# Kernel optimization log

Measured on AMD Instinct MI355X. Metric: run time of the kernel, lower is better.

## Reference

```python
import jax, jax.numpy as jnp
import numpy as np

N, F_IN, H, C, D, NH, L, FF = 4096, 256, 2, 64, 128, 4, 2, 2048
DEG = 32


def setup_inputs() -> dict:
    key = jax.random.key(0)
    ks = jax.random.split(key, 32)
    s = 0.05
    # graph: random edges + self loops (PyG GATConv adds self loops)
    src = jax.random.randint(ks[0], (N * DEG,), 0, N)
    dst = jax.random.randint(ks[1], (N * DEG,), 0, N)
    loop = jnp.arange(N)
    edge_index = jnp.stack([jnp.concatenate([src, loop]),
                            jnp.concatenate([dst, loop])]).astype(jnp.int64)
    inp = {
        'x': jax.random.normal(ks[2], (N, F_IN), jnp.float32),
        'edge_index': edge_index,
        'enc_w1': jax.random.normal(ks[3], (F_IN, 128), jnp.float32) * s,
        'enc_b1': jnp.zeros((128,), jnp.float32),
        'enc_w2': jax.random.normal(ks[4], (128, D), jnp.float32) * s,
        'enc_b2': jnp.zeros((D,), jnp.float32),
        'gat_w': jax.random.normal(ks[5], (D, H * C), jnp.float32) * s,
        'gat_asrc': jax.random.normal(ks[6], (H, C), jnp.float32) * s,
        'gat_adst': jax.random.normal(ks[7], (H, C), jnp.float32) * s,
        'gat_bias': jnp.zeros((H * C,), jnp.float32),
        't_wq': jax.random.normal(ks[8], (L, D, D), jnp.float32) * s,
        't_bq': jnp.zeros((L, D), jnp.float32),
        't_wk': jax.random.normal(ks[9], (L, D, D), jnp.float32) * s,
        't_bk': jnp.zeros((L, D), jnp.float32),
        't_wv': jax.random.normal(ks[10], (L, D, D), jnp.float32) * s,
        't_bv': jnp.zeros((L, D), jnp.float32),
        't_wo': jax.random.normal(ks[11], (L, D, D), jnp.float32) * s,
        't_bo': jnp.zeros((L, D), jnp.float32),
        't_ln1_g': jnp.ones((L, D), jnp.float32),
        't_ln1_b': jnp.zeros((L, D), jnp.float32),
        't_ln2_g': jnp.ones((L, D), jnp.float32),
        't_ln2_b': jnp.zeros((L, D), jnp.float32),
        't_w1': jax.random.normal(ks[12], (L, D, FF), jnp.float32) * s,
        't_b1': jnp.zeros((L, FF), jnp.float32),
        't_w2': jax.random.normal(ks[13], (L, FF, D), jnp.float32) * s,
        't_b2': jnp.zeros((L, D), jnp.float32),
    }
    return inp


def _layer_norm(v, g, b):
    m = v.mean(-1, keepdims=True)
    var = v.var(-1, keepdims=True)
    return (v - m) / jnp.sqrt(var + 1e-5) * g + b


def _forward(x, edge_index, enc_w1, enc_b1, enc_w2, enc_b2,
             gat_w, gat_asrc, gat_adst, gat_bias,
             t_wq, t_bq, t_wk, t_bk, t_wv, t_bv, t_wo, t_bo,
             t_ln1_g, t_ln1_b, t_ln2_g, t_ln2_b, t_w1, t_b1, t_w2, t_b2):
    n = x.shape[0]
    # encoder MLP: Linear -> ReLU -> Linear
    h = jnp.maximum(x @ enc_w1 + enc_b1, 0.0) @ enc_w2 + enc_b2  # [N, D]
    # GATConv (concat heads), dropout inactive (eval)
    heads, ch = gat_asrc.shape
    hh = (h @ gat_w).reshape(n, heads, ch)                       # [N, H, C]
    src, dst = edge_index[0], edge_index[1]
    a_src = (hh * gat_asrc).sum(-1)                              # [N, H]
    a_dst = (hh * gat_adst).sum(-1)
    e = jax.nn.leaky_relu(a_src[src] + a_dst[dst], 0.2)          # [E, H]
    # segment softmax over destination nodes
    e_max = jax.ops.segment_max(e, dst, num_segments=n)
    e_exp = jnp.exp(e - e_max[dst])
    denom = jax.ops.segment_sum(e_exp, dst, num_segments=n)
    alpha = e_exp / denom[dst]                                   # [E, H]
    agg = jax.ops.segment_sum(alpha[:, :, None] * hh[src], dst, num_segments=n)
    y = agg.reshape(n, heads * ch) + gat_bias                    # [N, D]
    # TransformerEncoder (post-LN, relu FFN), unbatched sequence of N nodes
    d = y.shape[-1]
    dh = d // NH
    for l in range(t_wq.shape[0]):
        q = (y @ t_wq[l] + t_bq[l]).reshape(n, NH, dh)
        k = (y @ t_wk[l] + t_bk[l]).reshape(n, NH, dh)
        v = (y @ t_wv[l] + t_bv[l]).reshape(n, NH, dh)
        scores = jnp.einsum('nhd,mhd->hnm', q, k) / jnp.sqrt(jnp.float32(dh))
        p = jax.nn.softmax(scores, axis=-1)
        a = jnp.einsum('hnm,mhd->nhd', p, v).reshape(n, d)
        a = a @ t_wo[l] + t_bo[l]
        y = _layer_norm(y + a, t_ln1_g[l], t_ln1_b[l])
        f = jnp.maximum(y @ t_w1[l] + t_b1[l], 0.0) @ t_w2[l] + t_b2[l]
        y = _layer_norm(y + f, t_ln2_g[l], t_ln2_b[l])
    return y


def reference(x, edge_index, enc_w1, enc_b1, enc_w2, enc_b2,
              gat_w, gat_asrc, gat_adst, gat_bias,
              t_wq, t_bq, t_wk, t_bk, t_wv, t_bv, t_wo, t_bo,
              t_ln1_g, t_ln1_b, t_ln2_g, t_ln2_b, t_w1, t_b1, t_w2, t_b2):
    return _forward(x, edge_index, enc_w1, enc_b1, enc_w2, enc_b2,
                    gat_w, gat_asrc, gat_adst, gat_bias,
                    t_wq, t_bq, t_wk, t_bk, t_wv, t_bv, t_wo, t_bo,
                    t_ln1_g, t_ln1_b, t_ln2_g, t_ln2_b, t_w1, t_b1, t_w2, t_b2)
```

## Files before the change

kernel.cpp:

```cpp
#include <hip/hip_runtime.h>

typedef unsigned short u16;
typedef unsigned int u32;
typedef __attribute__((ext_vector_type(8))) short bh8;
typedef __attribute__((ext_vector_type(4))) float fx4;
typedef __attribute__((ext_vector_type(4))) short s4;
typedef __attribute__((ext_vector_type(2))) unsigned int u32x2;

#define QS 0.2550437194342803f

__device__ __forceinline__ u16 f2bf(float f) {
    unsigned u = __float_as_uint(f);
    u += 0x7fffu + ((u >> 16) & 1u);
    return (u16)(u >> 16);
}

__device__ __forceinline__ u32 cvtpk(float lo, float hi) {
    u32 r;
    asm("v_cvt_pk_bf16_f32 %0, %1, %2" : "=v"(r) : "v"(lo), "v"(hi));
    return r;
}

__global__ __launch_bounds__(256) void prep_kernel(
    const float* x, const float* ew1, const float* ew2, const float* gw,
    const float* wq, const float* wk, const float* wv, const float* wo,
    const float* w1, const float* w2,
    const float* bq, const float* bk, const float* bv,
    u16* xb, u16* ew1t, u16* ew2t, u16* gwt,
    u16* wqkvt, float* bqkv, u16* wot, u16* w1t, u16* w2t)
{
    __shared__ u16 tile[64 * 65];
    int bid = blockIdx.x;
    const int t = threadIdx.x;

    if (bid < 128) {
        const float4* x4 = (const float4*)x;
        s4* o4 = (s4*)xb;
        #pragma unroll
        for (int i = 0; i < 8; i++) {
            int fi = bid * 2048 + i * 256 + t;
            float4 v = x4[fi];
            s4 o = { (short)f2bf(v.x), (short)f2bf(v.y), (short)f2bf(v.z), (short)f2bf(v.w) };
            o4[fi] = o;
        }
        return;
    }
    bid -= 128;
    if (bid < 1) {
        for (int idx = t; idx < 768; idx += 256) {
            int l = idx / 384, n = idx % 384;
            float v;
            if (n < 128)      v = bq[l * 128 + n] * QS;
            else if (n < 256) v = bk[l * 128 + n - 128];
            else              v = bv[l * 128 + n - 256];
            bqkv[idx] = v;
        }
        return;
    }
    bid -= 1;

    const float* src; u16* dst; int R, C, tr, tc; float sc = 1.f;
    if (bid < 8)            { src = ew1; dst = ew1t; R = 256; C = 128; tr = bid >> 1; tc = bid & 1; }
    else if ((bid -= 8) < 4)  { src = ew2; dst = ew2t; R = 128; C = 128; tr = bid >> 1; tc = bid & 1; }
    else if ((bid -= 4) < 4)  { src = gw;  dst = gwt;  R = 128; C = 128; tr = bid >> 1; tc = bid & 1; }
    else if ((bid -= 4) < 24) {
        int l = bid / 12, r2 = bid % 12, which = r2 >> 2, i = r2 & 3;
        R = 128; C = 128; tr = i >> 1; tc = i & 1;
        if (which == 0)      { src = wq + l * 16384; dst = wqkvt + l * 49152;         sc = QS; }
        else if (which == 1) { src = wk + l * 16384; dst = wqkvt + l * 49152 + 16384; }
        else                 { src = wv + l * 16384; dst = wqkvt + l * 49152 + 32768; }
    }
    else if ((bid -= 24) < 8)   { int l = bid >> 2, i = bid & 3;  src = wo + l * 16384; dst = wot + l * 16384; R = 128; C = 128; tr = i >> 1; tc = i & 1; }
    else if ((bid -= 8) < 128)  { int l = bid >> 6, i = bid & 63; src = w1 + (size_t)l * 262144; dst = w1t + (size_t)l * 262144; R = 128;  C = 2048; tr = i & 1;  tc = i >> 1; }
    else { bid -= 128;            int l = bid >> 6, i = bid & 63; src = w2 + (size_t)l * 262144; dst = w2t + (size_t)l * 262144; R = 2048; C = 128;  tr = i >> 1; tc = i & 1; }

    const int r = t >> 2, cs = (t & 3) * 16;
    const float* sp = src + (size_t)(tr * 64 + r) * C + tc * 64 + cs;
    #pragma unroll
    for (int j = 0; j < 16; j++) tile[r * 65 + cs + j] = f2bf(sp[j] * sc);
    __syncthreads();
    u16* dp = dst + (size_t)(tc * 64 + r) * R + tr * 64 + cs;
    #pragma unroll
    for (int j = 0; j < 16; j++) dp[j] = tile[(cs + j) * 65 + r];
}

__global__ __launch_bounds__(256) void gemm_bf16(
    const u16* __restrict__ A, const u16* __restrict__ Bt,
    const float* __restrict__ bias,
    float* __restrict__ Cf, u16* __restrict__ Cb, float* __restrict__ Cpart,
    u16* __restrict__ Cvt,
    int M, int N, int K, int relu, int kchunk, int ldc)
{
    __shared__ __align__(16) u16 As[2][64][40];
    __shared__ __align__(16) u16 Bs[2][64][40];
    const int m0 = blockIdx.x * 64, n0 = blockIdx.y * 64, z = blockIdx.z;
    const int tid = threadIdx.x;
    const int lane = tid & 63, w = tid >> 6;
    const int wm = (w >> 1) * 32, wn = (w & 1) * 32;
    const int l15 = lane & 15, l4 = lane >> 4;
    const int srow = tid >> 2, skq = (tid & 3) * 8;
    const int k0 = z * kchunk;

    const u16* Ap = A + (size_t)(m0 + srow) * K + k0 + skq;
    const u16* Bp = Bt + (size_t)(n0 + srow) * K + k0 + skq;

    fx4 acc00 = {0,0,0,0}, acc01 = {0,0,0,0}, acc10 = {0,0,0,0}, acc11 = {0,0,0,0};

    *(int4*)&As[0][srow][skq] = *(const int4*)Ap;
    *(int4*)&Bs[0][srow][skq] = *(const int4*)Bp;

    const int niter = kchunk >> 5;
    for (int it = 0; it < niter; it++) {
        const int cur = it & 1;
        int4 ar, br;
        __syncthreads();
        if (it + 1 < niter) {
            ar = *(const int4*)(Ap + (it + 1) * 32);
            br = *(const int4*)(Bp + (it + 1) * 32);
        }
        bh8 a0 = *(const bh8*)&As[cur][wm + l15][l4 * 8];
        bh8 a1 = *(const bh8*)&As[cur][wm + 16 + l15][l4 * 8];
        bh8 b0 = *(const bh8*)&Bs[cur][wn + l15][l4 * 8];
        bh8 b1 = *(const bh8*)&Bs[cur][wn + 16 + l15][l4 * 8];
        acc00 = __builtin_amdgcn_mfma_f32_16x16x32_bf16(a0, b0, acc00, 0, 0, 0);
        acc01 = __builtin_amdgcn_mfma_f32_16x16x32_bf16(a0, b1, acc01, 0, 0, 0);
        acc10 = __builtin_amdgcn_mfma_f32_16x16x32_bf16(a1, b0, acc10, 0, 0, 0);
        acc11 = __builtin_amdgcn_mfma_f32_16x16x32_bf16(a1, b1, acc11, 0, 0, 0);
        if (it + 1 < niter) {
            *(int4*)&As[cur ^ 1][srow][skq] = ar;
            *(int4*)&Bs[cur ^ 1][srow][skq] = br;
        }
    }

    fx4* accs[2][2] = {{&acc00, &acc01}, {&acc10, &acc11}};
    #pragma unroll
    for (int i = 0; i < 2; i++)
        #pragma unroll
        for (int j = 0; j < 2; j++) {
            int colg = n0 + wn + j * 16 + l15;
            int rowb = m0 + wm + i * 16 + l4 * 4;
            if (Cpart) {
                float* cp = Cpart + (size_t)z * M * N;
                #pragma unroll
                for (int r = 0; r < 4; r++)
                    cp[(size_t)(rowb + r) * N + colg] = (*accs[i][j])[r];
                continue;
            }
            float bvv = bias ? bias[colg] : 0.f;
            float vals[4];
            #pragma unroll
            for (int r = 0; r < 4; r++) {
                float v = (*accs[i][j])[r] + bvv;
                vals[r] = relu ? fmaxf(v, 0.f) : v;
            }
            if (Cvt && colg >= 256) {
                s4 pk = { (short)f2bf(vals[0]), (short)f2bf(vals[1]),
                          (short)f2bf(vals[2]), (short)f2bf(vals[3]) };
                *(s4*)&Cvt[(size_t)(colg - 256) * 4096 + rowb] = pk;
            } else {
                #pragma unroll
                for (int r = 0; r < 4; r++) {
                    if (Cf) Cf[(size_t)(rowb + r) * ldc + colg] = vals[r];
                    if (Cb) Cb[(size_t)(rowb + r) * ldc + colg] = f2bf(vals[r]);
                }
            }
        }
}

__global__ __launch_bounds__(128) void gat_prep(
    const float* __restrict__ hh, const float* __restrict__ asrc,
    const float* __restrict__ adst, float* __restrict__ an_src,
    float* __restrict__ an_dst)
{
    int n = blockIdx.x, tid = threadIdx.x;
    int head = tid >> 6, c = tid & 63;
    float v = hh[n * 128 + tid];
    float ps = v * asrc[head * 64 + c];
    float pd = v * adst[head * 64 + c];
    for (int off = 32; off; off >>= 1) { ps += __shfl_down(ps, off); pd += __shfl_down(pd, off); }
    if (c == 0) { an_src[n * 2 + head] = ps; an_dst[n * 2 + head] = pd; }
}

__global__ void count_edges(const int* __restrict__ dst, int* counts, int E) {
    int i = blockIdx.x * 256 + threadIdx.x;
    if (i < E) atomicAdd(&counts[dst[i]], 1);
}

__global__ __launch_bounds__(1024) void scan_kernel(const int* __restrict__ counts,
                                                    int* row_start, int* cursor) {
    __shared__ int s[1024];
    int tid = threadIdx.x, b = tid * 4;
    int c0 = counts[b], c1 = counts[b+1], c2 = counts[b+2], c3 = counts[b+3];
    int sum = c0 + c1 + c2 + c3;
    s[tid] = sum;
    __syncthreads();
    for (int off = 1; off < 1024; off <<= 1) {
        int v = (tid >= off) ? s[tid - off] : 0;
        __syncthreads();
        s[tid] += v;
        __syncthreads();
    }
    int excl = s[tid] - sum;
    int r0 = excl, r1 = excl + c0, r2 = r1 + c1, r3 = r2 + c2;
    row_start[b] = r0; row_start[b+1] = r1; row_start[b+2] = r2; row_start[b+3] = r3;
    cursor[b] = r0; cursor[b+1] = r1; cursor[b+2] = r2; cursor[b+3] = r3;
    if (tid == 1023) row_start[4096] = s[1023];
}

__global__ void scatter_edges(const int* __restrict__ src, const int* __restrict__ dst,
                              int* cursor, int* csr_src, int E) {
    int i = blockIdx.x * 256 + threadIdx.x;
    if (i < E) { int pos = atomicAdd(&cursor[dst[i]], 1); csr_src[pos] = src[i]; }
}

__global__ __launch_bounds__(256) void gat_aggregate(
    const int* __restrict__ row_start, const int* __restrict__ csr_src,
    const float* __restrict__ an_src, const float* __restrict__ an_dst,
    const float* __restrict__ hh, const float* __restrict__ gbias,
    float* __restrict__ y32, u16* __restrict__ yb)
{
    int n = blockIdx.x, tid = threadIdx.x;
    const int lane = tid & 63, wv = tid >> 6;
    int start = row_start[n], end = row_start[n + 1];
    float ad0 = an_dst[n * 2 + 0], ad1 = an_dst[n * 2 + 1];
    __shared__ float rmx[4][2], rsm[4][2];
    __shared__ float sal0[128], sal1[128], sagg[256];
    __shared__ int sidx[128];

    float mx0 = -1e30f, mx1 = -1e30f;
    for (int i = start + tid; i < end; i += 256) {
        int s = csr_src[i];
        float e0 = an_src[s * 2 + 0] + ad0; e0 = e0 > 0.f ? e0 : 0.2f * e0;
        float e1 = an_src[s * 2 + 1] + ad1; e1 = e1 > 0.f ? e1 : 0.2f * e1;
        mx0 = fmaxf(mx0, e0); mx1 = fmaxf(mx1, e1);
    }
    for (int off = 32; off; off >>= 1) { mx0 = fmaxf(mx0, __shfl_down(mx0, off)); mx1 = fmaxf(mx1, __shfl_down(mx1, off)); }
    if (lane == 0) { rmx[wv][0] = mx0; rmx[wv][1] = mx1; }
    __syncthreads();
    mx0 = fmaxf(fmaxf(rmx[0][0], rmx[1][0]), fmaxf(rmx[2][0], rmx[3][0]));
    mx1 = fmaxf(fmaxf(rmx[0][1], rmx[1][1]), fmaxf(rmx[2][1], rmx[3][1]));

    float den0 = 0.f, den1 = 0.f;
    for (int i = start + tid; i < end; i += 256) {
        int s = csr_src[i];
        float e0 = an_src[s * 2 + 0] + ad0; e0 = e0 > 0.f ? e0 : 0.2f * e0;
        float e1 = an_src[s * 2 + 1] + ad1; e1 = e1 > 0.f ? e1 : 0.2f * e1;
        den0 += __expf(e0 - mx0); den1 += __expf(e1 - mx1);
    }
    for (int off = 32; off; off >>= 1) { den0 += __shfl_down(den0, off); den1 += __shfl_down(den1, off); }
    if (lane == 0) { rsm[wv][0] = den0; rsm[wv][1] = den1; }
    __syncthreads();
    den0 = rsm[0][0] + rsm[1][0] + rsm[2][0] + rsm[3][0];
    den1 = rsm[0][1] + rsm[1][1] + rsm[2][1] + rsm[3][1];
    float rd0 = 1.f / den0, rd1 = 1.f / den1;

    const int grp = tid >> 7, ch = tid & 127, head = ch >> 6;
    float agg = 0.f;
    for (int c0 = start; c0 < end; c0 += 128) {
        int cnt = min(128, end - c0);
        __syncthreads();
        if (tid < cnt) {
            int s = csr_src[c0 + tid];
            float e0 = an_src[s * 2 + 0] + ad0; e0 = e0 > 0.f ? e0 : 0.2f * e0;
            float e1 = an_src[s * 2 + 1] + ad1; e1 = e1 > 0.f ? e1 : 0.2f * e1;
            sal0[tid] = __expf(e0 - mx0) * rd0;
            sal1[tid] = __expf(e1 - mx1) * rd1;
            sidx[tid] = s;
        }
        __syncthreads();
        const float* sal = head ? sal1 : sal0;
        for (int j = grp; j < cnt; j += 2)
            agg += sal[j] * hh[(size_t)sidx[j] * 128 + ch];
    }
    sagg[tid] = agg;
    __syncthreads();
    if (tid < 128) {
        float v = sagg[tid] + sagg[tid + 128] + gbias[tid];
        y32[(size_t)n * 128 + tid] = v;
        yb[(size_t)n * 128 + tid] = f2bf(v);
    }
}

__global__ __launch_bounds__(256) void flash_attn_part(
    const u16* __restrict__ q, const u16* __restrict__ k,
    const u16* __restrict__ vt, float* __restrict__ po,
    float* __restrict__ pm, float* __restrict__ pl)
{
    __shared__ __align__(16) u16 Kb[2][64][40];
    __shared__ __align__(16) u16 Vb[2][32][72];
    __shared__ __align__(16) u16 Ps[4][16][72];
    const int q0 = blockIdx.x * 64, h = blockIdx.y, ch = blockIdx.z;
    const int tid = threadIdx.x;
    const int w = tid >> 6, lane = tid & 63, l15 = lane & 15, l4 = lane >> 4;

    bh8 qf = *(const bh8*)&q[(size_t)(q0 + w * 16 + l15) * 256 + h * 32 + l4 * 8];

    const int skey = tid >> 2, sds = (tid & 3) * 8;
    const int svd = tid >> 3, svk = (tid & 7) * 8;
    const u16* kgp = &k[(size_t)(ch * 512 + skey) * 256 + h * 32 + sds];
    const u16* vgp = &vt[(size_t)(h * 32 + svd) * 4096 + ch * 512 + svk];

    fx4 o0 = {0,0,0,0}, o1 = {0,0,0,0};
    float M = -1e30f, L = 0.f;

    *(int4*)&Kb[0][skey][sds] = *(const int4*)kgp;
    *(int4*)&Vb[0][svd][svk] = *(const int4*)vgp;

    for (int ti = 0; ti < 8; ti++) {
        const int cur = ti & 1;
        int4 kr, vr;
        __syncthreads();
        if (ti < 7) {
            kr = *(const int4*)(kgp + (size_t)(ti + 1) * 64 * 256);
            vr = *(const int4*)(vgp + (ti + 1) * 64);
        }

        fx4 s[4];
        #pragma unroll
        for (int sub = 0; sub < 4; sub++) {
            bh8 kf = *(const bh8*)&Kb[cur][sub * 16 + l15][l4 * 8];
            fx4 z = {0,0,0,0};
            s[sub] = __builtin_amdgcn_mfma_f32_16x16x32_bf16(kf, qf, z, 0, 0, 0);
        }
        float t0 = fmaxf(fmaxf(s[0][0], s[0][1]), s[0][2]);
        float t1 = fmaxf(fmaxf(s[0][3], s[1][0]), s[1][1]);
        float t2 = fmaxf(fmaxf(s[1][2], s[1][3]), s[2][0]);
        float t3 = fmaxf(fmaxf(s[2][1], s[2][2]), s[2][3]);
        float t4 = fmaxf(fmaxf(s[3][0], s[3][1]), s[3][2]);
        float pmax = fmaxf(fmaxf(fmaxf(t0, t1), t2), fmaxf(fmaxf(t3, t4), s[3][3]));
        pmax = fmaxf(pmax, __shfl_xor(pmax, 16));
        pmax = fmaxf(pmax, __shfl_xor(pmax, 32));
        if (!__all(pmax - M <= 8.0f)) {
            float f = __builtin_amdgcn_exp2f(M - pmax);
            M = pmax;
            o0 *= f; o1 *= f; L *= f;
        }

        #pragma unroll
        for (int sub = 0; sub < 4; sub++)
            #pragma unroll
            for (int r = 0; r < 4; r++)
                s[sub][r] = __builtin_amdgcn_exp2f(s[sub][r] - M);
        float ss0 = (s[0][0] + s[0][1]) + (s[0][2] + s[0][3]);
        float ss1 = (s[1][0] + s[1][1]) + (s[1][2] + s[1][3]);
        float ss2 = (s[2][0] + s[2][1]) + (s[2][2] + s[2][3]);
        float ss3 = (s[3][0] + s[3][1]) + (s[3][2] + s[3][3]);
        float lsum = (ss0 + ss1) + (ss2 + ss3);
        lsum += __shfl_xor(lsum, 16);
        lsum += __shfl_xor(lsum, 32);
        L += lsum;

        #pragma unroll
        for (int sub = 0; sub < 4; sub++) {
            u32x2 pk = { cvtpk(s[sub][0], s[sub][1]), cvtpk(s[sub][2], s[sub][3]) };
            *(u32x2*)&Ps[w][l15][sub * 16 + l4 * 4] = pk;
        }

        #pragma unroll
        for (int kc = 0; kc < 2; kc++) {
            bh8 bf  = *(const bh8*)&Ps[w][l15][kc * 32 + l4 * 8];
            bh8 af0 = *(const bh8*)&Vb[cur][l15][kc * 32 + l4 * 8];
            bh8 af1 = *(const bh8*)&Vb[cur][16 + l15][kc * 32 + l4 * 8];
            o0 = __builtin_amdgcn_mfma_f32_16x16x32_bf16(af0, bf, o0, 0, 0, 0);
            o1 = __builtin_amdgcn_mfma_f32_16x16x32_bf16(af1, bf, o1, 0, 0, 0);
        }

        if (ti < 7) {
            *(int4*)&Kb[cur ^ 1][skey][sds] = kr;
            *(int4*)&Vb[cur ^ 1][svd][svk] = vr;
        }
    }
    const int base = (blockIdx.x * 4 + h) * 8 + ch;
    const int qrow = w * 16 + l15;
    *(fx4*)&po[(size_t)(base * 64 + qrow) * 32 + l4 * 4]      = o0;
    *(fx4*)&po[(size_t)(base * 64 + qrow) * 32 + 16 + l4 * 4] = o1;
    if (l4 == 0) { pm[base * 64 + qrow] = M; pl[base * 64 + qrow] = L; }
}

__global__ __launch_bounds__(256) void attn_combine(
    const float* __restrict__ po, const float* __restrict__ pm,
    const float* __restrict__ pl, u16* __restrict__ out)
{
    int qb = blockIdx.x, h = blockIdx.y;
    int col = threadIdx.x & 31, r0 = threadIdx.x >> 5;
    int rb = (qb * 4 + h) * 8;
    for (int j = 0; j < 8; j++) {
        int row = r0 * 8 + j;
        float m = -1e30f;
        for (int c = 0; c < 8; c++) m = fmaxf(m, pm[(rb + c) * 64 + row]);
        float l = 0.f, o = 0.f;
        for (int c = 0; c < 8; c++) {
            float wgt = __builtin_amdgcn_exp2f(pm[(rb + c) * 64 + row] - m);
            l += wgt * pl[(rb + c) * 64 + row];
            o += wgt * po[(size_t)((rb + c) * 64 + row) * 32 + col];
        }
        out[(size_t)(qb * 64 + row) * 128 + h * 32 + col] = f2bf(o / l);
    }
}

__global__ __launch_bounds__(128) void add_ln(
    const float* __restrict__ y, const float* __restrict__ delta,
    const float* __restrict__ g, const float* __restrict__ b,
    float* __restrict__ out32, u16* __restrict__ outb)
{
    int n = blockIdx.x, tid = threadIdx.x;
    float v = y[(size_t)n * 128 + tid] + delta[(size_t)n * 128 + tid];
    float sacc = v;
    for (int off = 32; off; off >>= 1) sacc += __shfl_down(sacc, off);
    __shared__ float sm[2], sv[2];
    if ((tid & 63) == 0) sm[tid >> 6] = sacc;
    __syncthreads();
    float mean = (sm[0] + sm[1]) * (1.f / 128.f);
    float d = v - mean;
    float qacc = d * d;
    for (int off = 32; off; off >>= 1) qacc += __shfl_down(qacc, off);
    if ((tid & 63) == 0) sv[tid >> 6] = qacc;
    __syncthreads();
    float var = (sv[0] + sv[1]) * (1.f / 128.f);
    float o = d * rsqrtf(var + 1e-5f) * g[tid] + b[tid];
    out32[(size_t)n * 128 + tid] = o;
    outb[(size_t)n * 128 + tid] = f2bf(o);
}

__global__ __launch_bounds__(128) void add_ln8(
    const float* __restrict__ y, const float* __restrict__ part,
    const float* __restrict__ bias,
    const float* __restrict__ g, const float* __restrict__ b,
    float* __restrict__ out32, u16* __restrict__ outb)
{
    int n = blockIdx.x, tid = threadIdx.x;
    float v = y[(size_t)n * 128 + tid] + bias[tid];
    for (int z = 0; z < 8; z++) v += part[(size_t)z * 524288 + n * 128 + tid];
    float sacc = v;
    for (int off = 32; off; off >>= 1) sacc += __shfl_down(sacc, off);
    __shared__ float sm[2], sv[2];
    if ((tid & 63) == 0) sm[tid >> 6] = sacc;
    __syncthreads();
    float mean = (sm[0] + sm[1]) * (1.f / 128.f);
    float d = v - mean;
    float qacc = d * d;
    for (int off = 32; off; off >>= 1) qacc += __shfl_down(qacc, off);
    if ((tid & 63) == 0) sv[tid >> 6] = qacc;
    __syncthreads();
    float var = (sv[0] + sv[1]) * (1.f / 128.f);
    float o = d * rsqrtf(var + 1e-5f) * g[tid] + b[tid];
    out32[(size_t)n * 128 + tid] = o;
    outb[(size_t)n * 128 + tid] = f2bf(o);
}

extern "C" void kernel_launch(void* const* d_in, const int* in_sizes, int n_in,
                              void* d_out, int out_size, void* d_ws, size_t ws_size,
                              hipStream_t stream)
{
    const float* x     = (const float*)d_in[0];
    const int*   ei    = (const int*)  d_in[1];
    const float* ew1   = (const float*)d_in[2];
    const float* eb1   = (const float*)d_in[3];
    const float* ew2   = (const float*)d_in[4];
    const float* eb2   = (const float*)d_in[5];
    const float* gw    = (const float*)d_in[6];
    const float* gasrc = (const float*)d_in[7];
    const float* gadst = (const float*)d_in[8];
    const float* gbias = (const float*)d_in[9];
    const float* wq    = (const float*)d_in[10];
    const float* bq    = (const float*)d_in[11];
    const float* wk    = (const float*)d_in[12];
    const float* bk    = (const float*)d_in[13];
    const float* wv    = (const float*)d_in[14];
    const float* bv    = (const float*)d_in[15];
    const float* wo    = (const float*)d_in[16];
    const float* bo    = (const float*)d_in[17];
    const float* ln1g  = (const float*)d_in[18];
    const float* ln1b  = (const float*)d_in[19];
    const float* ln2g  = (const float*)d_in[20];
    const float* ln2b  = (const float*)d_in[21];
    const float* w1    = (const float*)d_in[22];
    const float* b1    = (const float*)d_in[23];
    const float* w2    = (const float*)d_in[24];
    const float* b2    = (const float*)d_in[25];

    const int E = in_sizes[1] / 2;
    const int* esrc = ei;
    const int* edst = ei + E;

    char* p = (char*)d_ws;
    auto alloc = [&](size_t bytes) -> void* {
        void* r = (void*)p;
        p += (bytes + 255) & ~(size_t)255;
        return r;
    };
    u16* xb    = (u16*)alloc(4096 * 256 * 2);
    u16* ew1t  = (u16*)alloc(128 * 256 * 2);
    u16* ew2t  = (u16*)alloc(128 * 128 * 2);
    u16* gwt   = (u16*)alloc(128 * 128 * 2);
    u16* wqkvt = (u16*)alloc(2 * 384 * 128 * 2);
    float* bqkv = (float*)alloc(2 * 384 * 4);
    u16* wot   = (u16*)alloc(2 * 128 * 128 * 2);
    u16* w1t   = (u16*)alloc(2 * 2048 * 128 * 2);
    u16* w2t   = (u16*)alloc(2 * 128 * 2048 * 2);
    u16* h1b   = (u16*)alloc(4096 * 128 * 2);
    u16* hb    = (u16*)alloc(4096 * 128 * 2);
    float* hh  = (float*)alloc(4096 * 128 * 4);
    float* ansrc = (float*)alloc(4096 * 2 * 4);
    float* andst = (float*)alloc(4096 * 2 * 4);
    int* counts    = (int*)alloc(4096 * 4);
    int* row_start = (int*)alloc(4097 * 4);
    int* cursor    = (int*)alloc(4096 * 4);
    int* csr_src   = (int*)alloc((size_t)E * 4);
    float* y32 = (float*)alloc(4096 * 128 * 4);
    u16* yb    = (u16*)alloc(4096 * 128 * 2);
    u16* qkvb  = (u16*)alloc((size_t)4096 * 256 * 2);
    u16* vtb   = (u16*)alloc(4096 * 128 * 2);
    u16* attnb = (u16*)alloc(4096 * 128 * 2);
    float* po  = (float*)alloc((size_t)64 * 4 * 8 * 64 * 32 * 4);
    float* pm  = (float*)alloc(64 * 4 * 8 * 64 * 4);
    float* pl  = (float*)alloc(64 * 4 * 8 * 64 * 4);
    float* proj32 = (float*)alloc(4096 * 128 * 4);
    u16* ff1b  = (u16*)alloc((size_t)4096 * 2048 * 2);
    float* ff2part = (float*)alloc((size_t)8 * 4096 * 128 * 4);

    prep_kernel<<<433, 256, 0, stream>>>(x, ew1, ew2, gw, wq, wk, wv, wo, w1, w2,
                                         bq, bk, bv,
                                         xb, ew1t, ew2t, gwt, wqkvt, bqkv, wot, w1t, w2t);

    gemm_bf16<<<dim3(64, 2), 256, 0, stream>>>(xb, ew1t, eb1, nullptr, h1b, nullptr, nullptr, 4096, 128, 256, 1, 256, 128);
    gemm_bf16<<<dim3(64, 2), 256, 0, stream>>>(h1b, ew2t, eb2, nullptr, hb, nullptr, nullptr, 4096, 128, 128, 0, 128, 128);

    gemm_bf16<<<dim3(64, 2), 256, 0, stream>>>(hb, gwt, nullptr, hh, nullptr, nullptr, nullptr, 4096, 128, 128, 0, 128, 128);
    gat_prep<<<4096, 128, 0, stream>>>(hh, gasrc, gadst, ansrc, andst);
    hipMemsetAsync(counts, 0, 4096 * sizeof(int), stream);
    count_edges<<<(E + 255) / 256, 256, 0, stream>>>(edst, counts, E);
    scan_kernel<<<1, 1024, 0, stream>>>(counts, row_start, cursor);
    scatter_edges<<<(E + 255) / 256, 256, 0, stream>>>(esrc, edst, cursor, csr_src, E);
    gat_aggregate<<<4096, 256, 0, stream>>>(row_start, csr_src, ansrc, andst, hh, gbias, y32, yb);

    for (int l = 0; l < 2; l++) {
        gemm_bf16<<<dim3(64, 6), 256, 0, stream>>>(yb, wqkvt + l * 49152, bqkv + l * 384, nullptr, qkvb, nullptr, vtb, 4096, 384, 128, 0, 128, 256);
        flash_attn_part<<<dim3(64, 4, 8), 256, 0, stream>>>(qkvb, qkvb + 128, vtb, po, pm, pl);
        attn_combine<<<dim3(64, 4), 256, 0, stream>>>(po, pm, pl, attnb);
        gemm_bf16<<<dim3(64, 2), 256, 0, stream>>>(attnb, wot + l * 16384, bo + l * 128, proj32, nullptr, nullptr, nullptr, 4096, 128, 128, 0, 128, 128);
        add_ln<<<4096, 128, 0, stream>>>(y32, proj32, ln1g + l * 128, ln1b + l * 128, y32, yb);
        gemm_bf16<<<dim3(64, 32), 256, 0, stream>>>(yb, w1t + (size_t)l * 262144, b1 + l * 2048, nullptr, ff1b, nullptr, nullptr, 4096, 2048, 128, 1, 128, 2048);
        gemm_bf16<<<dim3(64, 2, 8), 256, 0, stream>>>(ff1b, w2t + (size_t)l * 262144, nullptr, nullptr, nullptr, ff2part, nullptr, 4096, 128, 2048, 0, 256, 128);
        float* outp = (l == 1) ? (float*)d_out : y32;
        add_ln8<<<4096, 128, 0, stream>>>(y32, ff2part, b2 + l * 128, ln2g + l * 128, ln2b + l * 128, outp, yb);
    }
}
```

Before: 209.8 us.

## Use wave-shuffle scan and halve flash attention key tile to 32

The scan kernel replaces its shared-memory Hillis-Steele loop, which needed many block barriers, with an intra-wave shuffle scan plus a small per-wave sum table and a single barrier. The flash attention partial kernel now processes 32 keys per iteration instead of 64 and runs twice as many iterations, using 8-byte global loads and smaller LDS buffers. This shrinks LDS footprint and register pressure, which may allow more resident blocks. In exchange it doubles the per-tile overhead: barriers, softmax max/sum shuffles and rescale checks.

```diff
diff --git a/kernel.cpp b/kernel.cpp
--- a/kernel.cpp
+++ b/kernel.cpp
@@ -188,23 +188,30 @@
 
 __global__ __launch_bounds__(1024) void scan_kernel(const int* __restrict__ counts,
                                                     int* row_start, int* cursor) {
-    __shared__ int s[1024];
-    int tid = threadIdx.x, b = tid * 4;
+    __shared__ int wsum[16];
+    int tid = threadIdx.x, lane = tid & 63, wv = tid >> 6;
+    int b = tid * 4;
     int c0 = counts[b], c1 = counts[b+1], c2 = counts[b+2], c3 = counts[b+3];
     int sum = c0 + c1 + c2 + c3;
-    s[tid] = sum;
-    __syncthreads();
-    for (int off = 1; off < 1024; off <<= 1) {
-        int v = (tid >= off) ? s[tid - off] : 0;
-        __syncthreads();
-        s[tid] += v;
-        __syncthreads();
-    }
-    int excl = s[tid] - sum;
+    int inc = sum;
+    #pragma unroll
+    for (int off = 1; off < 64; off <<= 1) {
+        int v = __shfl_up(inc, off);
+        if (lane >= off) inc += v;
+    }
+    if (lane == 63) wsum[wv] = inc;
+    __syncthreads();
+    int base = 0;
+    #pragma unroll
+    for (int i = 0; i < 16; i++) {
+        int v = wsum[i];
+        base += (i < wv) ? v : 0;
+    }
+    int excl = base + inc - sum;
     int r0 = excl, r1 = excl + c0, r2 = r1 + c1, r3 = r2 + c2;
     row_start[b] = r0; row_start[b+1] = r1; row_start[b+2] = r2; row_start[b+3] = r3;
     cursor[b] = r0; cursor[b+1] = r1; cursor[b+2] = r2; cursor[b+3] = r3;
-    if (tid == 1023) row_start[4096] = s[1023];
+    if (tid == 1023) row_start[4096] = base + inc;
 }
 
 __global__ void scatter_edges(const int* __restrict__ src, const int* __restrict__ dst,
@@ -286,48 +293,45 @@
     const u16* __restrict__ vt, float* __restrict__ po,
     float* __restrict__ pm, float* __restrict__ pl)
 {
-    __shared__ __align__(16) u16 Kb[2][64][40];
-    __shared__ __align__(16) u16 Vb[2][32][72];
-    __shared__ __align__(16) u16 Ps[4][16][72];
+    __shared__ __align__(16) u16 Kb[2][32][40];
+    __shared__ __align__(16) u16 Vb[2][32][40];
+    __shared__ __align__(16) u16 Ps[4][16][40];
     const int q0 = blockIdx.x * 64, h = blockIdx.y, ch = blockIdx.z;
     const int tid = threadIdx.x;
     const int w = tid >> 6, lane = tid & 63, l15 = lane & 15, l4 = lane >> 4;
 
     bh8 qf = *(const bh8*)&q[(size_t)(q0 + w * 16 + l15) * 256 + h * 32 + l4 * 8];
 
-    const int skey = tid >> 2, sds = (tid & 3) * 8;
-    const int svd = tid >> 3, svk = (tid & 7) * 8;
+    const int skey = tid >> 3, sds = (tid & 7) * 4;
+    const int svd = tid >> 3, svk = (tid & 7) * 4;
     const u16* kgp = &k[(size_t)(ch * 512 + skey) * 256 + h * 32 + sds];
     const u16* vgp = &vt[(size_t)(h * 32 + svd) * 4096 + ch * 512 + svk];
 
     fx4 o0 = {0,0,0,0}, o1 = {0,0,0,0};
     float M = -1e30f, L = 0.f;
 
-    *(int4*)&Kb[0][skey][sds] = *(const int4*)kgp;
-    *(int4*)&Vb[0][svd][svk] = *(const int4*)vgp;
-
-    for (int ti = 0; ti < 8; ti++) {
+    *(int2*)&Kb[0][skey][sds] = *(const int2*)kgp;
+    *(int2*)&Vb[0][svd][svk] = *(const int2*)vgp;
+
+    for (int ti = 0; ti < 16; ti++) {
         const int cur = ti & 1;
-        int4 kr, vr;
+        int2 kr, vr;
         __syncthreads();
-        if (ti < 7) {
-            kr = *(const int4*)(kgp + (size_t)(ti + 1) * 64 * 256);
-            vr = *(const int4*)(vgp + (ti + 1) * 64);
-        }
-
-        fx4 s[4];
+        if (ti < 15) {
+            kr = *(const int2*)(kgp + (size_t)(ti + 1) * 32 * 256);
+            vr = *(const int2*)(vgp + (ti + 1) * 32);
+        }
+
+        fx4 s[2];
         #pragma unroll
-        for (int sub = 0; sub < 4; sub++) {
+        for (int sub = 0; sub < 2; sub++) {
             bh8 kf = *(const bh8*)&Kb[cur][sub * 16 + l15][l4 * 8];
             fx4 z = {0,0,0,0};
             s[sub] = __builtin_amdgcn_mfma_f32_16x16x32_bf16(kf, qf, z, 0, 0, 0);
         }
-        float t0 = fmaxf(fmaxf(s[0][0], s[0][1]), s[0][2]);
-        float t1 = fmaxf(fmaxf(s[0][3], s[1][0]), s[1][1]);
-        float t2 = fmaxf(fmaxf(s[1][2], s[1][3]), s[2][0]);
-        float t3 = fmaxf(fmaxf(s[2][1], s[2][2]), s[2][3]);
-        float t4 = fmaxf(fmaxf(s[3][0], s[3][1]), s[3][2]);
-        float pmax = fmaxf(fmaxf(fmaxf(t0, t1), t2), fmaxf(fmaxf(t3, t4), s[3][3]));
+        float m0 = fmaxf(fmaxf(s[0][0], s[0][1]), fmaxf(s[0][2], s[0][3]));
+        float m1 = fmaxf(fmaxf(s[1][0], s[1][1]), fmaxf(s[1][2], s[1][3]));
+        float pmax = fmaxf(m0, m1);
         pmax = fmaxf(pmax, __shfl_xor(pmax, 16));
         pmax = fmaxf(pmax, __shfl_xor(pmax, 32));
         if (!__all(pmax - M <= 8.0f)) {
@@ -337,37 +341,34 @@
         }
 
         #pragma unroll
-        for (int sub = 0; sub < 4; sub++)
+        for (int sub = 0; sub < 2; sub++)
             #pragma unroll
             for (int r = 0; r < 4; r++)
                 s[sub][r] = __builtin_amdgcn_exp2f(s[sub][r] - M);
         float ss0 = (s[0][0] + s[0][1]) + (s[0][2] + s[0][3]);
         float ss1 = (s[1][0] + s[1][1]) + (s[1][2] + s[1][3]);
-        float ss2 = (s[2][0] + s[2][1]) + (s[2][2] + s[2][3]);
-        float ss3 = (s[3][0] + s[3][1]) + (s[3][2] + s[3][3]);
-        float lsum = (ss0 + ss1) + (ss2 + ss3);
+        float lsum = ss0 + ss1;
         lsum += __shfl_xor(lsum, 16);
         lsum += __shfl_xor(lsum, 32);
         L += lsum;
 
         #pragma unroll
-        for (int sub = 0; sub < 4; sub++) {
+        for (int sub = 0; sub < 2; sub++) {
             u32x2 pk = { cvtpk(s[sub][0], s[sub][1]), cvtpk(s[sub][2], s[sub][3]) };
             *(u32x2*)&Ps[w][l15][sub * 16 + l4 * 4] = pk;
         }
 
-        #pragma unroll
-        for (int kc = 0; kc < 2; kc++) {
-            bh8 bf  = *(const bh8*)&Ps[w][l15][kc * 32 + l4 * 8];
-            bh8 af0 = *(const bh8*)&Vb[cur][l15][kc * 32 + l4 * 8];
-            bh8 af1 = *(const bh8*)&Vb[cur][16 + l15][kc * 32 + l4 * 8];
+        {
+            bh8 bf  = *(const bh8*)&Ps[w][l15][l4 * 8];
+            bh8 af0 = *(const bh8*)&Vb[cur][l15][l4 * 8];
+            bh8 af1 = *(const bh8*)&Vb[cur][16 + l15][l4 * 8];
             o0 = __builtin_amdgcn_mfma_f32_16x16x32_bf16(af0, bf, o0, 0, 0, 0);
             o1 = __builtin_amdgcn_mfma_f32_16x16x32_bf16(af1, bf, o1, 0, 0, 0);
         }
 
-        if (ti < 7) {
-            *(int4*)&Kb[cur ^ 1][skey][sds] = kr;
-            *(int4*)&Vb[cur ^ 1][svd][svk] = vr;
+        if (ti < 15) {
+            *(int2*)&Kb[cur ^ 1][skey][sds] = kr;
+            *(int2*)&Vb[cur ^ 1][svd][svk] = vr;
         }
     }
     const int base = (blockIdx.x * 4 + h) * 8 + ch;
```

Result: slower. 215.2 us (+2.6%).
